# Performance work log

Hardware: AMD Instinct MI355X
Metric: run time of the kernel (lower is better)

Reference implementation:

```python
import jax, jax.numpy as jnp
import numpy as np

MASK_FILL = -1e-07  # faithful to original (tiny negative, not -1e7)


def setup_inputs() -> dict:
    key = jax.random.key(0)
    k1, k2, k3, k4 = jax.random.split(key, 4)
    B, L1, L2, D = 64, 1024, 1024, 256
    v1 = jax.random.normal(k1, (B, L1, D), dtype=jnp.float32)
    v2 = jax.random.normal(k2, (B, L2, D), dtype=jnp.float32)
    v1_mask = jax.random.randint(k3, (B, L1), 0, 2).astype(bool)  # True = pad
    v2_mask = jax.random.randint(k4, (B, L2), 0, 2).astype(bool)
    return {"v1": v1, "v1_mask": v1_mask, "v2": v2, "v2_mask": v2_mask}


def reference(v1, v1_mask, v2, v2_mask):
    # sim: [B, L1, L2]
    sim = jnp.einsum('bld,bmd->blm', v1, v2)
    # mask rows (pad positions of v1), then softmax over L1 (dim=1)
    sim1 = jnp.where(v1_mask[:, :, None], MASK_FILL, sim)
    v2_v1_attn = jax.nn.softmax(sim1, axis=1)
    # mask columns on the already row-masked matrix, softmax over L2 (dim=2)
    sim2 = jnp.where(v2_mask[:, None, :], MASK_FILL, sim1)
    v1_v2_attn = jax.nn.softmax(sim2, axis=2)
    attended_v1 = jnp.einsum('blm,bmd->bld', v1_v2_attn, v2)  # [B, L1, D]
    attended_v2 = jnp.einsum('blm,bld->bmd', v2_v1_attn, v1)  # [B, L2, D]
    attended_v1 = jnp.where(v1_mask[:, :, None], 0.0, attended_v1)
    attended_v2 = jnp.where(v2_mask[:, :, None], 0.0, attended_v2)
    return attended_v1, attended_v2
```

## Files before the change

### kernel.cpp

```cpp
#include <hip/hip_runtime.h>
#include <hip/hip_bf16.h>
#include <hip/hip_fp16.h>
#include <stdint.h>


#define MASK_FILL -1e-07f

typedef unsigned short u16;
typedef _Float16 half8 __attribute__((ext_vector_type(8)));
typedef __attribute__((ext_vector_type(4))) float f32x4;
typedef __attribute__((ext_vector_type(4))) u16 u16x4;

#define NB 64
#define LL 1024
#define DD 256
#define BQ 128
#define HB 32
#define ELEMS ((size_t)NB * LL * DD)
#define NIT_STREAM 128

__device__ __forceinline__ u16 f16b(float f) {
    _Float16 h = (_Float16)f;
    return __builtin_bit_cast(u16, h);
}
__device__ __forceinline__ unsigned pkf16(float a, float b) {
    return (unsigned)f16b(a) | ((unsigned)f16b(b) << 16);
}

__device__ __forceinline__ void gll16(const u16* g, u16* l) {
    __builtin_amdgcn_global_load_lds(
        (const __attribute__((address_space(1))) void*)g,
        (__attribute__((address_space(3))) void*)l, 16, 0, 0);
}

__global__ __launch_bounds__(256) void prep_masks(
    const void* __restrict__ m1, const void* __restrict__ m2,
    int* __restrict__ cm1, int* __restrict__ cm2,
    int* __restrict__ qidx1, int* __restrict__ pa1, int* __restrict__ qcnt1,
    int* __restrict__ qidx2, int* __restrict__ pa2, int* __restrict__ qcnt2,
    int* __restrict__ ctr)
{
    int blk = blockIdx.x, tid = threadIdx.x;
    int msk = blk >> 6, b = blk & 63;
    const unsigned* w1 = (const unsigned*)m1;
    const unsigned* w2 = (const unsigned*)m2;
    unsigned acc = 0;
    for (int i = tid; i < 4096; i += 256) acc |= (w1[i] | w2[i]) & ~1u;
    __shared__ unsigned red[256];
    red[tid] = acc;
    __syncthreads();
    for (int o = 128; o; o >>= 1) {
        if (tid < o) red[tid] |= red[tid + o];
        __syncthreads();
    }
    int isbool = red[0] ? 1 : 0;

    const void* m = msk ? m2 : m1;
    int* cm   = msk ? cm2 : cm1;
    int* qidx = msk ? qidx2 : qidx1;
    int* pa   = msk ? pa2 : pa1;
    int* qcnt = msk ? qcnt2 : qcnt1;

    __shared__ int ps[256];
    int f[4], s = 0;
#pragma unroll
    for (int j = 0; j < 4; ++j) {
        int idx = b * LL + tid * 4 + j;
        int v = isbool ? (int)((const unsigned char*)m)[idx] : ((const int*)m)[idx];
        cm[idx] = v ? 1 : 0;
        f[j] = (v == 0) ? 1 : 0;
        s += f[j];
    }
    ps[tid] = s;
    __syncthreads();
    for (int off = 1; off < 256; off <<= 1) {
        int v = (tid >= off) ? ps[tid - off] : 0;
        __syncthreads();
        ps[tid] += v;
        __syncthreads();
    }
    int pos = (tid > 0) ? ps[tid - 1] : 0;
#pragma unroll
    for (int j = 0; j < 4; ++j) {
        pa[b * LL + tid * 4 + j] = pos;
        if (f[j]) qidx[b * LL + (pos++)] = tid * 4 + j;
    }
    if (tid == 255) qcnt[b] = ps[255];
    if (blk == 0 && tid < 8) ctr[tid] = 0;
}

__global__ __launch_bounds__(256) void prep2_kernel(
    const float* __restrict__ x1, u16* __restrict__ h1, u16* __restrict__ t1,
    const int* __restrict__ cm1, const int* __restrict__ pa1,
    const int* __restrict__ qi1, const int* __restrict__ qc1,
    const float* __restrict__ x2, u16* __restrict__ h2, u16* __restrict__ t2,
    const int* __restrict__ cm2, const int* __restrict__ pa2,
    const int* __restrict__ qi2, const int* __restrict__ qc2,
    float* __restrict__ part, float* __restrict__ out)
{
    __shared__ u16 t[64][65];
    __shared__ float ps2[16][68];
    int blk = blockIdx.x;
    int tensor = blk >> 12;
    blk &= 4095;
    const float* x = tensor ? x2 : x1;
    u16* h  = tensor ? h2 : h1;
    u16* xt = tensor ? t2 : t1;
    const int* cm = tensor ? cm2 : cm1;
    const int* pa = tensor ? pa2 : pa1;
    const int* qi = tensor ? qi2 : qi1;
    const int* qc = tensor ? qc2 : qc1;
    float* outb = out + (tensor ? ELEMS : 0);
    int b = blk >> 6, lt = (blk >> 2) & 15, dt = blk & 3;
    int l0 = lt * 64, d0 = dt * 64;
    int tid = threadIdx.x;
    int sub = tid >> 4;
    int c16 = tid & 15;
    float vpart[4] = {0.f, 0.f, 0.f, 0.f};
#pragma unroll
    for (int p = 0; p < 4; ++p) {
        int row = p * 16 + sub;
        int l = l0 + row;
        int masked = cm[b * LL + l];
        int slot = pa[b * LL + l];
        f32x4 v = *(const f32x4*)(x + ((size_t)b * LL + l) * DD + d0 + c16 * 4);
        u16x4 hv;
#pragma unroll
        for (int e = 0; e < 4; ++e) {
            hv[e] = f16b(v[e]);
            t[c16 * 4 + e][row] = hv[e];
            if (masked) vpart[e] += v[e];
        }
        if (!masked) {
            *(u16x4*)(h + ((size_t)b * LL + slot) * DD + d0 + c16 * 4) = hv;
        } else {
            f32x4 z4 = {0.f, 0.f, 0.f, 0.f};
            *(f32x4*)(outb + ((size_t)b * LL + l) * DD + d0 + c16 * 4) = z4;
        }
    }
#pragma unroll
    for (int e = 0; e < 4; ++e) ps2[sub][c16 * 4 + e] = vpart[e];
    __syncthreads();
    int pos_base = pa[b * LL + l0];
    int cntb = qc[b];
    int nun = ((lt == 15) ? cntb : pa[b * LL + l0 + 64]) - pos_base;
#pragma unroll
    for (int p = 0; p < 4; ++p) {
        int d = p * 16 + sub;
#pragma unroll
        for (int e = 0; e < 4; ++e) {
            int j = c16 * 4 + e;
            if (j < nun) {
                int col = qi[b * LL + pos_base + j] - l0;
                xt[((size_t)b * DD + d0 + d) * LL + pos_base + j] = t[d][col];
            }
        }
    }
    if (tid < 64) {
        float s = 0.f;
#pragma unroll
        for (int k = 0; k < 16; ++k) s += ps2[k][tid];
        part[(((size_t)tensor * NB + b) * 16 + lt) * 256 + d0 + tid] = s;
    }
}

__global__ __launch_bounds__(256) void vsum_reduce(
    const float* __restrict__ part, float* __restrict__ vsum)
{
    int blk = blockIdx.x;
    int d = threadIdx.x;
    float s = 0.f;
#pragma unroll
    for (int lt = 0; lt < 16; ++lt)
        s += part[((size_t)blk * 16 + lt) * 256 + d];
    vsum[(size_t)blk * DD + d] = s;
}

__global__ __launch_bounds__(512, 2) void flash_fused(
    const u16* __restrict__ v1h, const u16* __restrict__ v2h,
    const u16* __restrict__ v1t, const u16* __restrict__ v2t,
    const int* __restrict__ qidx1, const int* __restrict__ qcnt1,
    const int* __restrict__ qidx2, const int* __restrict__ qcnt2,
    const float* __restrict__ vsum, int* __restrict__ ctr,
    float* __restrict__ out)
{
    int strm0 = blockIdx.x & 7;
    int tid = threadIdx.x;
    int w = tid >> 6, lane = tid & 63;
    int lq = lane & 15, g = lane >> 4;

    __shared__ __align__(16) u16 khs[2][2][HB * DD];
    __shared__ __align__(16) u16 vts[2][2][HB * DD];

    const int pvcc = (g ^ (lq & 3) ^ ((lq >> 2) & 3)) * 8;

#define STAGE(BUF, KT2)                                                         \
    {                                                                           \
        int k0s = (KT2) * 64;                                                   \
        _Pragma("unroll")                                                       \
        for (int t = 0; t < 8; ++t) {                                           \
            int u = t * 8 + w;                                                  \
            int n = u & 15;                                                     \
            int hh = (u >> 4) & 1;                                              \
            if (u < 32) {                                                       \
                unsigned phys = (unsigned)n * 1024u + (unsigned)lane * 16u;     \
                unsigned key = phys >> 9;                                       \
                unsigned cl = ((phys >> 4) & 31u) ^ (key & 7u);                 \
                size_t koff = kv_base + (size_t)(k0s + hh * HB + (int)key) * DD + cl * 8; \
                gll16(kh_g + koff, &khs[BUF][hh][n * 512]);                     \
            } else {                                                            \
                unsigned dv = (unsigned)n * 16u + ((unsigned)lane >> 2);        \
                unsigned cv = ((unsigned)lane & 3u) ^ (dv & 3u) ^ ((dv >> 2) & 3u); \
                size_t voff = vt_base + (size_t)dv * LL + (unsigned)(k0s + hh * HB) + cv * 8; \
                gll16(vt_g + voff, &vts[BUF][hh][n * 512]);                     \
            }                                                                   \
        }                                                                       \
    }

    for (int ss = 0; ss < 8; ++ss) {
        int s2 = (strm0 + ss) & 7;
        for (;;) {
            __syncthreads();
            if (tid == 0) *(int*)&khs[0][0][0] = atomicAdd(&ctr[s2], 1);
            __syncthreads();
            int it = *(const int*)&khs[0][0][0];
            __syncthreads();
            if (it >= NIT_STREAM) break;
            int qt  = it & 7;
            int dir = (it >> 3) & 1;
            int b   = ((it >> 4) << 3) + s2;

            const u16 *qh_g, *kh_g, *vt_g;
            const int *qidx, *qcq, *qck;
            const float* vsp;
            float* ob;
            if (dir == 0) { qh_g=v1h; kh_g=v2h; vt_g=v2t;
                            qidx=qidx1; qcq=qcnt1; qck=qcnt2;
                            vsp = vsum + ((size_t)NB + b) * DD; ob = out; }
            else          { qh_g=v2h; kh_g=v1h; vt_g=v1t;
                            qidx=qidx2; qcq=qcnt2; qck=qcnt1;
                            vsp = vsum + (size_t)b * DD; ob = out + ELEMS; }
            int cnt_q = qcq[b];
            if (qt * BQ >= cnt_q) continue;
            int cnt_k = qck[b];
            int nkt2 = (cnt_k + 63) >> 6;

            int qslot = qt * BQ + w * 16 + lq;
            bool qvalid = qslot < cnt_q;

            const u16* qbh = qh_g + ((size_t)b * LL + qslot) * DD + g * 8;
            half8 qhf[8];
#pragma unroll
            for (int ks = 0; ks < 8; ++ks)
                qhf[ks] = *(const half8*)(const void*)(qbh + ks * 32);

            float m = MASK_FILL, z = 0.f;
            f32x4 o[16];
#pragma unroll
            for (int i2 = 0; i2 < 16; ++i2) o[i2] = (f32x4){0.f, 0.f, 0.f, 0.f};

            const size_t kv_base = (size_t)b * LL * DD;
            const size_t vt_base = (size_t)b * DD * LL;

            if (nkt2 > 0) {
                int cur = 0;
                STAGE(0, 0);
                asm volatile("s_waitcnt vmcnt(0)" ::: "memory");
                __builtin_amdgcn_s_barrier();
                __builtin_amdgcn_sched_barrier(0);

                for (int kt2 = 0; kt2 < nkt2; ++kt2) {
                    int k0 = kt2 * 64;
                    if (kt2 + 1 < nkt2) STAGE(cur ^ 1, kt2 + 1);

                    f32x4 sa[2][2];
#pragma unroll
                    for (int hh = 0; hh < 2; ++hh)
#pragma unroll
                        for (int rt = 0; rt < 2; ++rt)
                            sa[hh][rt] = (f32x4){0.f, 0.f, 0.f, 0.f};
                    __builtin_amdgcn_s_setprio(1);
#pragma unroll
                    for (int hh = 0; hh < 2; ++hh) {
#pragma unroll
                        for (int ks = 0; ks < 8; ++ks) {
                            int cidx = ((ks * 4 + g) ^ (lq & 7)) * 8;
                            half8 kh0 = *(const half8*)(const void*)&khs[cur][hh][lq * 256 + cidx];
                            half8 kh1 = *(const half8*)(const void*)&khs[cur][hh][(16 + lq) * 256 + cidx];
                            sa[hh][0] = __builtin_amdgcn_mfma_f32_16x16x32_f16(kh0, qhf[ks], sa[hh][0], 0, 0, 0);
                            sa[hh][1] = __builtin_amdgcn_mfma_f32_16x16x32_f16(kh1, qhf[ks], sa[hh][1], 0, 0, 0);
                        }
                    }
                    __builtin_amdgcn_s_setprio(0);

                    float s[16];
#pragma unroll
                    for (int hh = 0; hh < 2; ++hh)
#pragma unroll
                        for (int i2 = 0; i2 < 4; ++i2) {
                            s[hh * 8 + i2]     = sa[hh][0][i2];
                            s[hh * 8 + 4 + i2] = sa[hh][1][i2];
                        }
                    if (kt2 == nkt2 - 1) {
#pragma unroll
                        for (int hh = 0; hh < 2; ++hh) {
                            int base = k0 + hh * HB + 4 * g;
#pragma unroll
                            for (int i2 = 0; i2 < 4; ++i2) {
                                if (base + i2 >= cnt_k)      s[hh * 8 + i2]     = -1e30f;
                                if (base + 16 + i2 >= cnt_k) s[hh * 8 + 4 + i2] = -1e30f;
                            }
                        }
                    }
                    float pmax = s[0];
#pragma unroll
                    for (int i2 = 1; i2 < 16; ++i2) pmax = fmaxf(pmax, s[i2]);
                    pmax = fmaxf(pmax, __shfl_xor(pmax, 16));
                    pmax = fmaxf(pmax, __shfl_xor(pmax, 32));
                    if (__any(pmax > m)) {
                        float mnew = fmaxf(m, pmax);
                        float alpha = __expf(m - mnew);
                        z *= alpha;
#pragma unroll
                        for (int i2 = 0; i2 < 16; ++i2) o[i2] *= alpha;
                        m = mnew;
                    }
                    float p[16], psum = 0.f;
#pragma unroll
                    for (int i2 = 0; i2 < 16; ++i2) { p[i2] = __expf(s[i2] - m); psum += p[i2]; }
                    psum += __shfl_xor(psum, 16);
                    psum += __shfl_xor(psum, 32);
                    z += psum;

                    union { unsigned u[4]; half8 v; } pf[2];
                    int srcA = ((lane & 16) << 1) | lq;
                    int srcB = srcA + 16;
                    bool sel = (g >> 1) != 0;
#pragma unroll
                    for (int hh = 0; hh < 2; ++hh) {
                        unsigned pk00 = pkf16(p[hh * 8 + 0], p[hh * 8 + 1]);
                        unsigned pk01 = pkf16(p[hh * 8 + 2], p[hh * 8 + 3]);
                        unsigned pk10 = pkf16(p[hh * 8 + 4], p[hh * 8 + 5]);
                        unsigned pk11 = pkf16(p[hh * 8 + 6], p[hh * 8 + 7]);
                        unsigned a00 = (unsigned)__shfl((int)pk00, srcA);
                        unsigned a01 = (unsigned)__shfl((int)pk01, srcA);
                        unsigned a10 = (unsigned)__shfl((int)pk10, srcA);
                        unsigned a11 = (unsigned)__shfl((int)pk11, srcA);
                        unsigned b00 = (unsigned)__shfl((int)pk00, srcB);
                        unsigned b01 = (unsigned)__shfl((int)pk01, srcB);
                        unsigned b10 = (unsigned)__shfl((int)pk10, srcB);
                        unsigned b11 = (unsigned)__shfl((int)pk11, srcB);
                        pf[hh].u[0] = sel ? a10 : a00;
                        pf[hh].u[1] = sel ? a11 : a01;
                        pf[hh].u[2] = sel ? b10 : b00;
                        pf[hh].u[3] = sel ? b11 : b01;
                    }

                    __builtin_amdgcn_s_setprio(1);
#pragma unroll
                    for (int dt = 0; dt < 16; ++dt) {
                        int d = dt * 16 + lq;
                        half8 vf0 = *(const half8*)(const void*)&vts[cur][0][d * 32 + pvcc];
                        half8 vf1 = *(const half8*)(const void*)&vts[cur][1][d * 32 + pvcc];
                        o[dt] = __builtin_amdgcn_mfma_f32_16x16x32_f16(vf0, pf[0].v, o[dt], 0, 0, 0);
                        o[dt] = __builtin_amdgcn_mfma_f32_16x16x32_f16(vf1, pf[1].v, o[dt], 0, 0, 0);
                    }
                    __builtin_amdgcn_s_setprio(0);

                    if (kt2 + 1 < nkt2) {
                        asm volatile("s_waitcnt vmcnt(0)" ::: "memory");
                        __builtin_amdgcn_s_barrier();
                        __builtin_amdgcn_sched_barrier(0);
                    }
                    cur ^= 1;
                }
            }

            float wl = __expf(MASK_FILL - m);
            z += (float)(LL - cnt_k) * wl;
#pragma unroll
            for (int dt = 0; dt < 16; ++dt) {
                f32x4 vv = *(const f32x4*)(vsp + dt * 16 + 4 * g);
                o[dt] += wl * vv;
            }

            if (qvalid) {
                int qrow = qidx[b * LL + qslot];
                float zinv = 1.0f / z;
                float* orow = ob + ((size_t)b * LL + qrow) * DD + 4 * g;
#pragma unroll
                for (int dt = 0; dt < 16; ++dt) {
                    f32x4 vv = o[dt] * zinv;
                    *(f32x4*)(orow + dt * 16) = vv;
                }
            }
        }
    }
#undef STAGE
}

extern "C" void kernel_launch(void* const* d_in, const int* in_sizes, int n_in,
                              void* d_out, int out_size, void* d_ws, size_t ws_size,
                              hipStream_t stream)
{
    const float* v1      = (const float*)d_in[0];
    const void*  v1_mask = d_in[1];
    const float* v2      = (const float*)d_in[2];
    const void*  v2_mask = d_in[3];
    float* out = (float*)d_out;

    u16* v1h = (u16*)d_ws;
    u16* v2h = v1h + ELEMS;
    u16* v1t = v2h + ELEMS;
    u16* v2t = v1t + ELEMS;
    int* qidx1 = (int*)(v2t + ELEMS);
    int* qcnt1 = qidx1 + NB * LL;
    int* qidx2 = qcnt1 + NB;
    int* qcnt2 = qidx2 + NB * LL;
    int* cm1   = qcnt2 + NB;
    int* cm2   = cm1 + NB * LL;
    int* pa1   = cm2 + NB * LL;
    int* pa2   = pa1 + NB * LL;
    int* ctr   = pa2 + NB * LL;
    float* part = (float*)(ctr + 16);
    float* vsum = part + 2 * NB * 16 * 256;

    prep_masks<<<dim3(128), dim3(256), 0, stream>>>(
        v1_mask, v2_mask, cm1, cm2,
        qidx1, pa1, qcnt1, qidx2, pa2, qcnt2, ctr);

    prep2_kernel<<<dim3(2 * NB * 64), dim3(256), 0, stream>>>(
        v1, v1h, v1t, cm1, pa1, qidx1, qcnt1,
        v2, v2h, v2t, cm2, pa2, qidx2, qcnt2, part, out);
    vsum_reduce<<<dim3(2 * NB), dim3(256), 0, stream>>>(part, vsum);

    flash_fused<<<dim3(256), dim3(512), 0, stream>>>(
        v1h, v2h, v1t, v2t,
        qidx1, qcnt1, qidx2, qcnt2, vsum, ctr, out);
}
```

Measured before the change: 213.1 us.

## Vectorize transposed scatter writes and prefetch V fragments before softmax

The transpose-scatter epilogue now groups output slots into aligned quads and writes four f16 values with one vector store. Scalar stores remain only for the partial quads at the edges. In the attention loop, half of the V fragments are loaded from LDS into registers before the softmax math, so those LDS reads can overlap the exp and shuffle work ahead of the PV MFMAs. The prefetch holds sixteen extra half8 registers, which raises register pressure and may reduce occupancy.

```diff
diff --git a/kernel.cpp b/kernel.cpp
--- a/kernel.cpp
+++ b/kernel.cpp
@@ -141,18 +141,36 @@
 #pragma unroll
     for (int e = 0; e < 4; ++e) ps2[sub][c16 * 4 + e] = vpart[e];
     __syncthreads();
-    int pos_base = pa[b * LL + l0];
+    int first = pa[b * LL + l0];
     int cntb = qc[b];
-    int nun = ((lt == 15) ? cntb : pa[b * LL + l0 + 64]) - pos_base;
+    int nun = ((lt == 15) ? cntb : pa[b * LL + l0 + 64]) - first;
+    int last = first + nun;
+    int q0 = first >> 2;
+    int nq = ((last + 3) >> 2) - q0;
+    const int* qib = qi + b * LL;
 #pragma unroll
     for (int p = 0; p < 4; ++p) {
         int d = p * 16 + sub;
-#pragma unroll
-        for (int e = 0; e < 4; ++e) {
-            int j = c16 * 4 + e;
-            if (j < nun) {
-                int col = qi[b * LL + pos_base + j] - l0;
-                xt[((size_t)b * DD + d0 + d) * LL + pos_base + j] = t[d][col];
+        u16* xrow = xt + ((size_t)b * DD + d0 + d) * LL;
+        for (int qq = c16; qq < nq; qq += 16) {
+            int s0 = (q0 + qq) << 2;
+            if (s0 >= first && s0 + 4 <= last) {
+                u16x4 ov;
+#pragma unroll
+                for (int e = 0; e < 4; ++e) {
+                    int col = qib[s0 + e] - l0;
+                    ov[e] = t[d][col];
+                }
+                *(u16x4*)(xrow + s0) = ov;
+            } else {
+#pragma unroll
+                for (int e = 0; e < 4; ++e) {
+                    int sl = s0 + e;
+                    if (sl >= first && sl < last) {
+                        int col = qib[sl] - l0;
+                        xrow[sl] = t[d][col];
+                    }
+                }
             }
         }
     }
@@ -293,6 +311,14 @@
                     }
                     __builtin_amdgcn_s_setprio(0);
 
+                    half8 vfA[8], vfB[8];
+#pragma unroll
+                    for (int dt = 0; dt < 8; ++dt) {
+                        int d = dt * 16 + lq;
+                        vfA[dt] = *(const half8*)(const void*)&vts[cur][0][d * 32 + pvcc];
+                        vfB[dt] = *(const half8*)(const void*)&vts[cur][1][d * 32 + pvcc];
+                    }
+
                     float s[16];
 #pragma unroll
                     for (int hh = 0; hh < 2; ++hh)
@@ -358,7 +384,12 @@
 
                     __builtin_amdgcn_s_setprio(1);
 #pragma unroll
-                    for (int dt = 0; dt < 16; ++dt) {
+                    for (int dt = 0; dt < 8; ++dt) {
+                        o[dt] = __builtin_amdgcn_mfma_f32_16x16x32_f16(vfA[dt], pf[0].v, o[dt], 0, 0, 0);
+                        o[dt] = __builtin_amdgcn_mfma_f32_16x16x32_f16(vfB[dt], pf[1].v, o[dt], 0, 0, 0);
+                    }
+#pragma unroll
+                    for (int dt = 8; dt < 16; ++dt) {
                         int d = dt * 16 + lq;
                         half8 vf0 = *(const half8*)(const void*)&vts[cur][0][d * 32 + pvcc];
                         half8 vf1 = *(const half8*)(const void*)&vts[cur][1][d * 32 + pvcc];
```

New measurement: 208.6 us. 1.02x faster.
